# Kernel tuning notes

Hardware: AMD Instinct MI355X
Metric: run time of the kernel (lower is better)

The kernel has to match this reference:

```python
import jax, jax.numpy as jnp
import numpy as np

TAU = 250.0   # tau_inv used by all behaviours (norse default / explicit for LLBN)
DT = 0.001
VTH = 30.0
T_STEPS = 10000

# (a, b, c, d) Izhikevich params per cell
LLBN_P = (0.1, -0.075, -55.0, 6.0)      # custom spiking behaviour
EBN_P = (0.02, 0.25, -55.0, 0.05)       # phasic_bursting
IFN_P = (0.02, 0.25, -65.0, 6.0)        # phasic_spiking
TN_P = (0.02, 0.2, -65.0, 6.0)          # tonic_spiking
MN_P = (0.02, 0.25, -65.0, 6.0)         # phasic_spiking


def setup_inputs() -> dict:
    key = jax.random.key(0)
    k1, k2 = jax.random.split(key)
    input_mat = jax.random.uniform(k1, (127, 127), dtype=jnp.float32)
    weights_matrix = jax.random.uniform(k2, (12,), dtype=jnp.float32)
    return {"input_mat": input_mat, "weights_matrix": weights_matrix,
            "nb_repetitions": T_STEPS}


def _izh(v, u, I, p):
    a, b, c, d = p
    v1 = v + TAU * DT * (0.04 * v * v + 5.0 * v + 140.0 - u + I)
    u1 = u + TAU * DT * a * (b * v - u)
    z = (v1 >= VTH).astype(v.dtype)
    return z, jnp.where(z > 0, c, v1), u1 + z * d


def _simulate(input_mat, w, nb_repetitions):
    z_plus = jnp.sum(input_mat * w[0])  # constant across timesteps

    def step(carry, _):
        temp, z2p, v2, u2, v3, u3, v4, u4, z5p, v5, u5, v6, u6 = carry
        # LLBN: recurrent cell, input current = w2*(z_plus*w1 - temp) + w3*z_prev
        z2, v2, u2 = _izh(v2, u2, w[2] * (z_plus * w[1] - temp) + w[3] * z2p, LLBN_P)
        # EBN
        z3, v3, u3 = _izh(v3, u3, z_plus * w[4] + z2 * w[5], EBN_P)
        # IFN (feedback to LLBN via temp, one-step delay)
        z4, v4, u4 = _izh(v4, u4, z3 * w[6], IFN_P)
        temp_n = z4 * w[7]
        # TN: recurrent cell, input current = w9*(z3*w8) + w10*z_prev
        z5, v5, u5 = _izh(v5, u5, w[9] * (z3 * w[8]) + w[10] * z5p, TN_P)
        # MN
        z6, v6, u6 = _izh(v6, u6, z5 * w[11], MN_P)
        new_carry = (temp_n, z2, v2, u2, v3, u3, v4, u4, z5, v5, u5, v6, u6)
        out = (jnp.stack([z2, z3, z4, z5, z6]),  # spikes [5]
               jnp.stack([v2, v3, v4, v5, v6]))  # membrane voltages [5]
        return new_carry, out

    f32 = jnp.float32
    init = (f32(0.0),                      # temp
            f32(0.0), f32(-60.0), f32(4.5),    # LLBN z, v, u (u0 = b*v_rest)
            f32(-64.0), f32(-16.0),            # EBN v, u
            f32(-64.0), f32(-16.0),            # IFN v, u
            f32(0.0), f32(-70.0), f32(-14.0),  # TN z, v, u
            f32(-64.0), f32(-16.0))            # MN v, u
    _, (spikes, volts) = jax.lax.scan(step, init, None, length=nb_repetitions)
    return spikes.T, volts.T  # each [5, T]


def reference(input_mat, weights_matrix, nb_repetitions):
    o_spikes, v = _simulate(input_mat, weights_matrix, nb_repetitions)
    return o_spikes, v
```

## Files before the change

### kernel.cpp

```cpp
#include <hip/hip_runtime.h>

#pragma clang fp contract(off)


__device__ __forceinline__ float sel_mask(float a, float b, unsigned long long m) {
    float r;
    asm("v_cndmask_b32 %0, %1, %2, %3" : "=v"(r) : "v"(a), "v"(b), "s"(m));
    return r;
}

__global__ __launch_bounds__(256) void net_sim(const float* __restrict__ mat,
                                               const float* __restrict__ w,
                                               float* __restrict__ out,
                                               int* __restrict__ ws,
                                               int T) {
    __shared__ double red[256];
    const int tid = threadIdx.x;

    const float w0 = w[0];
    double s = 0.0;
    for (int i = tid; i < 127 * 127; i += 256) {
        float p = mat[i] * w0;
        s += (double)p;
    }
    red[tid] = s;
    __syncthreads();
    #pragma unroll
    for (int off = 128; off > 0; off >>= 1) {
        if (tid < off) red[tid] += red[tid + off];
        __syncthreads();
    }
    if (tid >= 9) return;

    const float z_plus = (float)red[0];

    const float w2 = w[2], w3 = w[3], w5 = w[5], w6 = w[6], w7 = w[7],
                w8 = w[8], w9 = w[9], w10 = w[10], w11 = w[11];
    const float zp_w1 = z_plus * w[1];
    const float zp_w4 = z_plus * w[4];

    const float I2_00 = w2 * (zp_w1 - 0.0f) + w3 * 0.0f;
    const float I2_10 = w2 * (zp_w1 - 0.0f) + w3 * 1.0f;
    const float I2_01 = w2 * (zp_w1 - w7)   + w3 * 0.0f;
    const float I2_11 = w2 * (zp_w1 - w7)   + w3 * 1.0f;
    const float I3_0  = zp_w4 + 0.0f * w5;
    const float I3_1  = zp_w4 + 1.0f * w5;
    const float I4_0  = 0.0f * w6;
    const float I4_1  = 1.0f * w6;
    const float I5_00 = w9 * (0.0f * w8) + w10 * 0.0f;
    const float I5_10 = w9 * (1.0f * w8) + w10 * 0.0f;
    const float I5_01 = w9 * (0.0f * w8) + w10 * 1.0f;
    const float I5_11 = w9 * (1.0f * w8) + w10 * 1.0f;
    const float I6_0  = 0.0f * w11;
    const float I6_1  = 1.0f * w11;

    const int lane = tid;
    const int g = lane == 0 ? 0 : lane <= 2 ? 1 : lane <= 4 ? 2 : lane <= 6 ? 3 : 4;

    const float ka = lane == 0 ? (float)(0.25 * 0.1) : (float)(0.25 * 0.02);
    const float b  = lane == 0 ? -0.075f : (g == 3 ? 0.2f : 0.25f);
    const float c  = g <= 1 ? -55.0f : -65.0f;
    const float d  = g == 1 ? 0.05f : 6.0f;
    float v = g == 0 ? -60.0f : (g == 3 ? -70.0f : -64.0f);
    float u = g == 0 ? 4.5f   : (g == 3 ? -14.0f : -16.0f);

    const float C0a = g == 0 ? I2_00 : g == 1 ? I3_0 : g == 2 ? I4_0
                    : g == 3 ? I5_00 : I6_0;
    const float C0b = g == 0 ? I2_00 : g == 1 ? I3_0 : g == 2 ? I4_0
                    : g == 3 ? I5_01 : I6_0;
    const float C1a = g == 1 ? I3_1 : g == 2 ? I4_1 : g == 3 ? I5_10
                    : g == 4 ? I6_1 : 0.0f;
    const float C1b = g == 1 ? I3_1 : g == 2 ? I4_1 : g == 3 ? I5_11
                    : g == 4 ? I6_1 : 0.0f;

    const bool is_lane0  = (lane == 0);
    const bool spec_var1 = (lane == 2) | (lane == 4) | (lane == 6) | (lane == 8);

    float* __restrict__ psp = out + g * T;
    float* __restrict__ pvv = out + 5 * T + g * T;

    int z2 = 0, z4 = 0, z5 = 0;

    float rav = 0.0f, rau = 0.0f; int raz2 = 0, raz4 = 0, raz5 = 0, ra_t = -1;
    float cav = 0.0f, cau = 0.0f; int caz2 = 0, caz4 = 0, caz5 = 0, ca_t = -1;
    int next_coarse = 8;
    int t_det = -1, Pf = 0;
    int blk5 = 0;

    float zb[8], vb[8];

    int t = 0;
    for (; t + 8 <= T; t += 8) {
        if (blk5 == 0) {
            if (ra_t >= 0) {
                unsigned long long mv =
                    __ballot(__float_as_uint(v) == __float_as_uint(rav));
                unsigned long long mu =
                    __ballot(__float_as_uint(u) == __float_as_uint(rau));
                if (((mv & mu) & 0x1FFull) == 0x1FFull &&
                    z2 == raz2 && z4 == raz4 && z5 == raz5) {
                    t_det = t; Pf = t - ra_t;
                    break;
                }
            }
            if (t) { rav = v; rau = u; raz2 = z2; raz4 = z4; raz5 = z5; ra_t = t; }
        } else if (ca_t >= 0) {
            unsigned long long mv =
                __ballot(__float_as_uint(v) == __float_as_uint(cav));
            unsigned long long mu =
                __ballot(__float_as_uint(u) == __float_as_uint(cau));
            if (((mv & mu) & 0x1FFull) == 0x1FFull &&
                z2 == caz2 && z4 == caz4 && z5 == caz5) {
                t_det = t; Pf = t - ca_t;
                break;
            }
        }
        if (t == next_coarse) {
            cav = v; cau = u; caz2 = z2; caz4 = z4; caz5 = z5; ca_t = t;
            next_coarse <<= 1;
        }
        blk5 = (blk5 == 4) ? 0 : (blk5 + 1);

        #pragma unroll
        for (int j = 0; j < 8; ++j) {
            float fI2 = z4 ? (z2 ? I2_11 : I2_01) : (z2 ? I2_10 : I2_00);
            float V0 = z5 ? C0b : C0a;
            float V1 = z5 ? C1b : C1a;
            V0 = is_lane0 ? fI2 : V0;
            float Ib = spec_var1 ? V1 : V0;

            float t1 = 0.04f * v;
            float t2 = t1 * v;
            float t3 = 5.0f * v;
            float t4 = t2 + t3;
            float t5 = t4 + 140.0f;
            float t6 = t5 - u;
            float bv = b * v;
            float bvu = bv - u;
            float du = ka * bvu;
            float u1 = u + du;

            float t7b = t6 + Ib;
            float dvb = 0.25f * t7b;
            float v1b = v + dvb;
            unsigned long long m = __ballot(v1b >= 30.0f);

            int nz2 = (int)(m & 1ull);
            int z3  = (int)((m >> (1 + nz2)) & 1ull);
            int nz4 = (int)((m >> (3 + z3)) & 1ull);
            int nz5 = (int)((m >> (5 + z3)) & 1ull);
            unsigned long long ssel =
                (nz2 ? 0x006ull : 0ull) | (z3 ? 0x078ull : 0ull)
              | (nz5 ? 0x180ull : 0ull);

            float Ia = sel_mask(V0, V1, ssel);
            float t7a = t6 + Ia;
            float dva = 0.25f * t7a;
            float v1a = v + dva;
            bool fa = (v1a >= 30.0f);
            v = fa ? c : v1a;
            float u1d = u1 + d;
            u = fa ? u1d : u1;

            zb[j] = fa ? 1.0f : 0.0f;
            vb[j] = v;

            z2 = nz2; z4 = nz4; z5 = nz5;
        }
        *(float4*)(psp)     = make_float4(zb[0], zb[1], zb[2], zb[3]);
        *(float4*)(psp + 4) = make_float4(zb[4], zb[5], zb[6], zb[7]);
        *(float4*)(pvv)     = make_float4(vb[0], vb[1], vb[2], vb[3]);
        *(float4*)(pvv + 4) = make_float4(vb[4], vb[5], vb[6], vb[7]);
        psp += 8;
        pvv += 8;
    }
    for (; t < T && t_det < 0; ++t) {
        float fI2 = z4 ? (z2 ? I2_11 : I2_01) : (z2 ? I2_10 : I2_00);
        float V0 = z5 ? C0b : C0a;
        float V1 = z5 ? C1b : C1a;
        V0 = is_lane0 ? fI2 : V0;
        float Ib = spec_var1 ? V1 : V0;
        float t1 = 0.04f * v;
        float t2 = t1 * v;
        float t3 = 5.0f * v;
        float t4 = t2 + t3;
        float t5 = t4 + 140.0f;
        float t6 = t5 - u;
        float bv = b * v;
        float bvu = bv - u;
        float du = ka * bvu;
        float u1 = u + du;
        float t7b = t6 + Ib;
        float dvb = 0.25f * t7b;
        float v1b = v + dvb;
        unsigned long long m = __ballot(v1b >= 30.0f);
        int nz2 = (int)(m & 1ull);
        int z3  = (int)((m >> (1 + nz2)) & 1ull);
        int nz4 = (int)((m >> (3 + z3)) & 1ull);
        int nz5 = (int)((m >> (5 + z3)) & 1ull);
        unsigned long long ssel =
            (nz2 ? 0x006ull : 0ull) | (z3 ? 0x078ull : 0ull)
          | (nz5 ? 0x180ull : 0ull);
        float Ia = sel_mask(V0, V1, ssel);
        float t7a = t6 + Ia;
        float dva = 0.25f * t7a;
        float v1a = v + dva;
        bool fa = (v1a >= 30.0f);
        v = fa ? c : v1a;
        float u1d = u1 + d;
        u = fa ? u1d : u1;
        psp[0] = fa ? 1.0f : 0.0f;
        pvv[0] = v;
        ++psp; ++pvv;
        z2 = nz2; z4 = nz4; z5 = nz5;
    }

    if (lane == 0) {
        ws[0] = (t_det >= 0) ? 1 : 0;
        ws[1] = t_det;
        ws[2] = Pf;
    }
}

__global__ __launch_bounds__(256) void fill_cycle(float* __restrict__ out,
                                                  const int* __restrict__ ws,
                                                  int T) {
    if (ws[0] == 0) return;
    const int t0 = ws[1];
    const int P  = ws[2];
    const int r  = blockIdx.y;
    const float* __restrict__ src = out + (size_t)r * T + (t0 - P);
    float* __restrict__ dst       = out + (size_t)r * T + t0;
    const int n = T - t0;
    for (int i = blockIdx.x * blockDim.x + threadIdx.x; i < n;
         i += gridDim.x * blockDim.x) {
        dst[i] = src[i % P];
    }
}

extern "C" void kernel_launch(void* const* d_in, const int* in_sizes, int n_in,
                              void* d_out, int out_size, void* d_ws, size_t ws_size,
                              hipStream_t stream) {
    const float* mat = (const float*)d_in[0];
    const float* w   = (const float*)d_in[1];
    int T = out_size / 10;
    net_sim<<<1, 256, 0, stream>>>(mat, w, (float*)d_out, (int*)d_ws, T);
    dim3 grid(40, 10, 1);
    fill_cycle<<<grid, 256, 0, stream>>>((float*)d_out, (const int*)d_ws, T);
}
```

Baseline: 300.9 us.

## Use DPP lane-swap pairs for speculative spike branches instead of second evaluation

Lanes are re-laid out so each speculative pair (input 0 / input 1) sits in adjacent lanes, and the LLBN moves to lane 8. Each step now computes one voltage update per lane plus a single ballot. A DPP quad-perm swap fetches the partner's result, replacing the old two-phase scheme that did a ballot and then a second voltage evaluation with a mask select. This shortens the serial per-step dependency chain but adds a DPP op, extra selects, and some scalar bit extraction per step.

Measured after the change: 295.9 us. Within noise of the previous version (-1.6%).

```diff
diff --git a/kernel.cpp b/kernel.cpp
--- a/kernel.cpp
+++ b/kernel.cpp
@@ -3,10 +3,9 @@
 #pragma clang fp contract(off)
 
 
-__device__ __forceinline__ float sel_mask(float a, float b, unsigned long long m) {
-    float r;
-    asm("v_cndmask_b32 %0, %1, %2, %3" : "=v"(r) : "v"(a), "v"(b), "s"(m));
-    return r;
+__device__ __forceinline__ float dpp_swap1(float x) {
+    return __int_as_float(__builtin_amdgcn_update_dpp(
+        0, __float_as_int(x), 0xB1, 0xF, 0xF, true));
 }
 
 __global__ __launch_bounds__(256) void net_sim(const float* __restrict__ mat,
@@ -55,26 +54,24 @@
     const float I6_1  = 1.0f * w11;
 
     const int lane = tid;
-    const int g = lane == 0 ? 0 : lane <= 2 ? 1 : lane <= 4 ? 2 : lane <= 6 ? 3 : 4;
-
-    const float ka = lane == 0 ? (float)(0.25 * 0.1) : (float)(0.25 * 0.02);
-    const float b  = lane == 0 ? -0.075f : (g == 3 ? 0.2f : 0.25f);
-    const float c  = g <= 1 ? -55.0f : -65.0f;
-    const float d  = g == 1 ? 0.05f : 6.0f;
-    float v = g == 0 ? -60.0f : (g == 3 ? -70.0f : -64.0f);
-    float u = g == 0 ? 4.5f   : (g == 3 ? -14.0f : -16.0f);
-
-    const float C0a = g == 0 ? I2_00 : g == 1 ? I3_0 : g == 2 ? I4_0
-                    : g == 3 ? I5_00 : I6_0;
-    const float C0b = g == 0 ? I2_00 : g == 1 ? I3_0 : g == 2 ? I4_0
-                    : g == 3 ? I5_01 : I6_0;
-    const float C1a = g == 1 ? I3_1 : g == 2 ? I4_1 : g == 3 ? I5_10
-                    : g == 4 ? I6_1 : 0.0f;
-    const float C1b = g == 1 ? I3_1 : g == 2 ? I4_1 : g == 3 ? I5_11
-                    : g == 4 ? I6_1 : 0.0f;
-
-    const bool is_lane0  = (lane == 0);
-    const bool spec_var1 = (lane == 2) | (lane == 4) | (lane == 6) | (lane == 8);
+    const bool isLLBN = (lane == 8);
+    const bool isTN   = ((lane >> 1) == 2);
+    const int g = isLLBN ? 0 : 1 + (lane >> 1);
+    const unsigned lane_bit = 1u << lane;
+
+    const float ka = isLLBN ? (float)(0.25 * 0.1) : (float)(0.25 * 0.02);
+    const float b  = isLLBN ? -0.075f : (isTN ? 0.2f : 0.25f);
+    const float c  = (isLLBN || g == 1) ? -55.0f : -65.0f;
+    const float d  = (g == 1) ? 0.05f : 6.0f;
+    float v = isLLBN ? -60.0f : (isTN ? -70.0f : -64.0f);
+    float u = isLLBN ? 4.5f   : (isTN ? -14.0f : -16.0f);
+
+    const float Ib_a =
+        lane == 0 ? I3_0 : lane == 1 ? I3_1 :
+        lane == 2 ? I4_0 : lane == 3 ? I4_1 :
+        lane == 4 ? I5_00 : lane == 5 ? I5_10 :
+        lane == 6 ? I6_0 : lane == 7 ? I6_1 : I2_00;
+    const float Ib_b = lane == 4 ? I5_01 : lane == 5 ? I5_11 : Ib_a;
 
     float* __restrict__ psp = out + g * T;
     float* __restrict__ pvv = out + 5 * T + g * T;
@@ -124,10 +121,8 @@
         #pragma unroll
         for (int j = 0; j < 8; ++j) {
             float fI2 = z4 ? (z2 ? I2_11 : I2_01) : (z2 ? I2_10 : I2_00);
-            float V0 = z5 ? C0b : C0a;
-            float V1 = z5 ? C1b : C1a;
-            V0 = is_lane0 ? fI2 : V0;
-            float Ib = spec_var1 ? V1 : V0;
+            float Ibs = z5 ? Ib_b : Ib_a;
+            float Ib  = isLLBN ? fI2 : Ibs;
 
             float t1 = 0.04f * v;
             float t2 = t1 * v;
@@ -139,30 +134,33 @@
             float bvu = bv - u;
             float du = ka * bvu;
             float u1 = u + du;
-
-            float t7b = t6 + Ib;
-            float dvb = 0.25f * t7b;
-            float v1b = v + dvb;
-            unsigned long long m = __ballot(v1b >= 30.0f);
-
-            int nz2 = (int)(m & 1ull);
-            int z3  = (int)((m >> (1 + nz2)) & 1ull);
-            int nz4 = (int)((m >> (3 + z3)) & 1ull);
-            int nz5 = (int)((m >> (5 + z3)) & 1ull);
-            unsigned long long ssel =
-                (nz2 ? 0x006ull : 0ull) | (z3 ? 0x078ull : 0ull)
-              | (nz5 ? 0x180ull : 0ull);
-
-            float Ia = sel_mask(V0, V1, ssel);
-            float t7a = t6 + Ia;
-            float dva = 0.25f * t7a;
-            float v1a = v + dva;
-            bool fa = (v1a >= 30.0f);
-            v = fa ? c : v1a;
             float u1d = u1 + d;
-            u = fa ? u1d : u1;
-
-            zb[j] = fa ? 1.0f : 0.0f;
+
+            float t7 = t6 + Ib;
+            float dv = 0.25f * t7;
+            float v1 = v + dv;
+            float v1p = dpp_swap1(v1);
+            bool fa  = (v1  >= 30.0f);
+            bool fap = (v1p >= 30.0f);
+            unsigned long long m = __ballot(fa);
+
+            unsigned mlo = (unsigned)m;
+            int nz2 = (int)((mlo >> 8) & 1u);
+            int z3  = nz2 ? (int)((mlo >> 1) & 1u) : (int)(mlo & 1u);
+            int nz4 = z3 ? (int)((mlo >> 3) & 1u) : (int)((mlo >> 2) & 1u);
+            int nz5 = z3 ? (int)((mlo >> 5) & 1u) : (int)((mlo >> 4) & 1u);
+            unsigned pm32 = (nz2 ? 0x01u : 0x02u)
+                          | (z3  ? 0x14u : 0x28u)
+                          | (nz5 ? 0x40u : 0x80u);
+            bool take_p = (pm32 & lane_bit) != 0u;
+
+            float wv  = fa  ? c : v1;
+            float wvp = fap ? c : v1p;
+            float uc  = fa  ? u1d : u1;
+            float ucp = fap ? u1d : u1;
+            v = take_p ? wvp : wv;
+            u = take_p ? ucp : uc;
+            zb[j] = take_p ? (fap ? 1.0f : 0.0f) : (fa ? 1.0f : 0.0f);
             vb[j] = v;
 
             z2 = nz2; z4 = nz4; z5 = nz5;
@@ -176,10 +174,8 @@
     }
     for (; t < T && t_det < 0; ++t) {
         float fI2 = z4 ? (z2 ? I2_11 : I2_01) : (z2 ? I2_10 : I2_00);
-        float V0 = z5 ? C0b : C0a;
-        float V1 = z5 ? C1b : C1a;
-        V0 = is_lane0 ? fI2 : V0;
-        float Ib = spec_var1 ? V1 : V0;
+        float Ibs = z5 ? Ib_b : Ib_a;
+        float Ib  = isLLBN ? fI2 : Ibs;
         float t1 = 0.04f * v;
         float t2 = t1 * v;
         float t3 = 5.0f * v;
@@ -190,26 +186,30 @@
         float bvu = bv - u;
         float du = ka * bvu;
         float u1 = u + du;
-        float t7b = t6 + Ib;
-        float dvb = 0.25f * t7b;
-        float v1b = v + dvb;
-        unsigned long long m = __ballot(v1b >= 30.0f);
-        int nz2 = (int)(m & 1ull);
-        int z3  = (int)((m >> (1 + nz2)) & 1ull);
-        int nz4 = (int)((m >> (3 + z3)) & 1ull);
-        int nz5 = (int)((m >> (5 + z3)) & 1ull);
-        unsigned long long ssel =
-            (nz2 ? 0x006ull : 0ull) | (z3 ? 0x078ull : 0ull)
-          | (nz5 ? 0x180ull : 0ull);
-        float Ia = sel_mask(V0, V1, ssel);
-        float t7a = t6 + Ia;
-        float dva = 0.25f * t7a;
-        float v1a = v + dva;
-        bool fa = (v1a >= 30.0f);
-        v = fa ? c : v1a;
         float u1d = u1 + d;
-        u = fa ? u1d : u1;
-        psp[0] = fa ? 1.0f : 0.0f;
+        float t7 = t6 + Ib;
+        float dv = 0.25f * t7;
+        float v1 = v + dv;
+        float v1p = dpp_swap1(v1);
+        bool fa  = (v1  >= 30.0f);
+        bool fap = (v1p >= 30.0f);
+        unsigned long long m = __ballot(fa);
+        unsigned mlo = (unsigned)m;
+        int nz2 = (int)((mlo >> 8) & 1u);
+        int z3  = nz2 ? (int)((mlo >> 1) & 1u) : (int)(mlo & 1u);
+        int nz4 = z3 ? (int)((mlo >> 3) & 1u) : (int)((mlo >> 2) & 1u);
+        int nz5 = z3 ? (int)((mlo >> 5) & 1u) : (int)((mlo >> 4) & 1u);
+        unsigned pm32 = (nz2 ? 0x01u : 0x02u)
+                      | (z3  ? 0x14u : 0x28u)
+                      | (nz5 ? 0x40u : 0x80u);
+        bool take_p = (pm32 & lane_bit) != 0u;
+        float wv  = fa  ? c : v1;
+        float wvp = fap ? c : v1p;
+        float uc  = fa  ? u1d : u1;
+        float ucp = fap ? u1d : u1;
+        v = take_p ? wvp : wv;
+        u = take_p ? ucp : uc;
+        psp[0] = take_p ? (fap ? 1.0f : 0.0f) : (fa ? 1.0f : 0.0f);
         pvv[0] = v;
         ++psp; ++pvv;
         z2 = nz2; z4 = nz4; z5 = nz5;
```
